# Kernel optimization log

Measured on AMD Instinct MI355X. Metric: run time of the kernel, lower is better.

The kernel has to match this reference:

```python
import jax, jax.numpy as jnp
import numpy as np

NUM_EMBEDDINGS = 1024
EMBEDDING_DIM = 256
COMMITMENT_COST = 0.25
DECAY = 0.99
EPSILON = 1e-05


def setup_inputs() -> dict:
    key = jax.random.key(0)
    k1, k2, k3 = jax.random.split(key, 3)
    z = jax.random.normal(k1, (32, EMBEDDING_DIM, 32, 32), dtype=jnp.float32)
    codebook = jax.random.normal(k2, (NUM_EMBEDDINGS, EMBEDDING_DIM), dtype=jnp.float32)
    ema_cluster_size = jnp.zeros((NUM_EMBEDDINGS,), dtype=jnp.float32)
    ema_dw = jax.random.normal(k3, (NUM_EMBEDDINGS, EMBEDDING_DIM), dtype=jnp.float32)
    return {"z": z, "codebook": codebook, "ema_cluster_size": ema_cluster_size, "ema_dw": ema_dw}


def reference(z, codebook, ema_cluster_size, ema_dw):
    K, D = codebook.shape
    # (B,C,H,W) -> (B,H,W,C)
    zp = jnp.transpose(z, (0, 2, 3, 1))
    z_flat = zp.reshape(-1, D)  # [N, D]
    N = z_flat.shape[0]

    # squared L2 distances to each code: [N, K]
    distances = (jnp.sum(z_flat ** 2, axis=1, keepdims=True)
                 + jnp.sum(codebook ** 2, axis=1)
                 - 2.0 * z_flat @ codebook.T)
    idx = jnp.argmin(distances, axis=1)  # [N]

    quantized = codebook[idx].reshape(zp.shape)  # [B,H,W,C]

    # training-mode EMA codebook update (one-hot scatter expressed as segment sums)
    counts = jax.ops.segment_sum(jnp.ones((N,), z_flat.dtype), idx, num_segments=K)  # encodings.sum(0)
    dw = jax.ops.segment_sum(z_flat, idx, num_segments=K)                            # encodings.T @ z_flat
    new_cluster_size = ema_cluster_size * DECAY + (1.0 - DECAY) * counts
    new_ema_dw = ema_dw * DECAY + (1.0 - DECAY) * dw
    n = jnp.sum(new_cluster_size)
    cluster_size = (new_cluster_size + EPSILON) / (n + K * EPSILON) * n
    new_codebook = new_ema_dw / cluster_size[:, None]

    commitment_loss = jnp.mean((zp - jax.lax.stop_gradient(quantized)) ** 2)
    loss = COMMITMENT_COST * commitment_loss

    # straight-through estimator
    quantized_st = zp + jax.lax.stop_gradient(quantized - zp)

    avg_probs = counts / N
    perplexity = jnp.exp(-jnp.sum(avg_probs * jnp.log(avg_probs + 1e-10)))

    quantized_out = jnp.transpose(quantized_st, (0, 3, 1, 2))  # back to (B,C,H,W)
    return (quantized_out, loss, perplexity, new_codebook, new_cluster_size, new_ema_dw)
```

## Files before the change

### kernel.cpp

```cpp
#include <hip/hip_runtime.h>
#include <cfloat>
#include <cstdint>

#define B_BATCH 32
#define D_DIM   256
#define HW      1024
#define N_POS   32768
#define K_CODES 1024
#define DECAY_F   0.99f
#define ONE_M_DECAY 0.01f
#define EPS_F   1e-5f

#define OUT_Q    0
#define OUT_LOSS 8388608
#define OUT_PERP 8388609
#define OUT_CB   8388610
#define OUT_NCS  8650754
#define OUT_EDW  8651778


#define WS_COUNTS  0
#define WS_LOSS    4096
#define WS_NTOT    4100
#define WS_MEMSET  4104
#define WS_CBNORM  4352
#define WS_OFFS    8448
#define WS_CURSOR  12544
#define WS_IDX     16640
#define WS_SORTED  147712
#define WS_CBHI    278784
#define WS_CBLO    803072
#define WS_PART    1327360
#define WS_SCODE   3424512
#define WS_TOTAL   3555584

typedef short s16x8 __attribute__((ext_vector_type(8)));
typedef float f32x4 __attribute__((ext_vector_type(4)));
typedef unsigned long long u64;

__device__ __forceinline__ ushort f2bf_rne(float x) {
    uint u = __float_as_uint(x);
    uint r = (u + 0x7FFF + ((u >> 16) & 1)) >> 16;
    return (ushort)r;
}
__device__ __forceinline__ float bf2f(ushort h) {
    return __uint_as_float(((uint)h) << 16);
}

__device__ __forceinline__ void gload16(const void* g, void* l) {
    __builtin_amdgcn_global_load_lds(
        (const __attribute__((address_space(1))) unsigned*)(uintptr_t)g,
        (__attribute__((address_space(3))) unsigned*)(uintptr_t)l, 16, 0, 0);
}

__global__ __launch_bounds__(256) void prep_kernel(const float* __restrict__ cb,
                                                   ushort* __restrict__ hi,
                                                   ushort* __restrict__ lo,
                                                   float* __restrict__ cbnorm) {
    int wave = threadIdx.x >> 6;
    int lane = threadIdx.x & 63;
    int k = blockIdx.x * 4 + wave;
    float4 v = *(const float4*)&cb[(size_t)k * D_DIM + lane * 4];
    ushort4 h, l;
    h.x = f2bf_rne(v.x); l.x = f2bf_rne(v.x - bf2f(h.x));
    h.y = f2bf_rne(v.y); l.y = f2bf_rne(v.y - bf2f(h.y));
    h.z = f2bf_rne(v.z); l.z = f2bf_rne(v.z - bf2f(h.z));
    h.w = f2bf_rne(v.w); l.w = f2bf_rne(v.w - bf2f(h.w));
    *(ushort4*)&hi[(size_t)k * D_DIM + lane * 4] = h;
    *(ushort4*)&lo[(size_t)k * D_DIM + lane * 4] = l;
    float s = v.x * v.x + v.y * v.y + v.z * v.z + v.w * v.w;
    #pragma unroll
    for (int off = 32; off >= 1; off >>= 1) s += __shfl_xor(s, off);
    if (lane == 0) cbnorm[k] = s;
}

__global__ __launch_bounds__(256) void ztrans_kernel(const float* __restrict__ z,
                                                     ushort* __restrict__ zhi,
                                                     ushort* __restrict__ zlo) {
    __shared__ float Zs[32][65];
    const int tid = threadIdx.x;
    const int n0  = blockIdx.x * 64;
    const int b   = n0 >> 10;
    const int hw0 = n0 & 1023;
    const float* zb = z + (size_t)b * (D_DIM * HW) + hw0;

    const int zn = tid & 63;
    const int zdb = (tid >> 6) * 8;
    const int n  = tid >> 2;
    const int dq = tid & 3;

    for (int d0 = 0; d0 < D_DIM; d0 += 32) {
        __syncthreads();
        #pragma unroll
        for (int j = 0; j < 8; ++j)
            Zs[zdb + j][zn] = zb[(size_t)(d0 + zdb + j) * HW + zn];
        __syncthreads();
        s16x8 hv, lv;
        #pragma unroll
        for (int j = 0; j < 8; ++j) {
            float f = Zs[dq * 8 + j][n];
            ushort hb = f2bf_rne(f);
            ushort lb = f2bf_rne(f - bf2f(hb));
            hv[j] = (short)hb;
            lv[j] = (short)lb;
        }
        *(s16x8*)&zhi[(size_t)(n0 + n) * D_DIM + d0 + dq * 8] = hv;
        *(s16x8*)&zlo[(size_t)(n0 + n) * D_DIM + d0 + dq * 8] = lv;
    }
}

__global__ __launch_bounds__(256) void argmin_gemm(const ushort* __restrict__ cbhi,
                                                   const ushort* __restrict__ cblo,
                                                   const ushort* __restrict__ zhi,
                                                   const ushort* __restrict__ zlo,
                                                   const float* __restrict__ cbnorm,
                                                   u64* __restrict__ partial) {
    __shared__ ushort lds[16384];
    __shared__ u64 kred[128][2];

    const int tid  = threadIdx.x;
    const int wave = tid >> 6;
    const int lane = tid & 63;
    const int col  = lane & 15;
    const int lg   = lane >> 4;
    const int mt = blockIdx.x & 7;
    const int pt = blockIdx.x >> 3;
    const int ch = wave & 1;
    const int ph = wave >> 1;

    const int r0  = tid >> 2;
    const int dch = (tid & 3) ^ ((r0 >> 1) & 3);
    const size_t eA0 = (size_t)(mt * 128 + r0) * D_DIM + dch * 8;
    const size_t eB0 = (size_t)(pt * 128 + r0) * D_DIM + dch * 8;
    const int ldsw = wave * 512;

    const int swz = (lg ^ ((col >> 1) & 3)) * 8;
    const int soffA = (ch * 64 + col) * 32 + swz;
    const int soffB = (ph * 64 + col) * 32 + swz;

    f32x4 acc[4][4];
    #pragma unroll
    for (int mi = 0; mi < 4; ++mi)
        #pragma unroll
        for (int ni = 0; ni < 4; ++ni) acc[mi][ni] = {0.f, 0.f, 0.f, 0.f};

    for (int s8 = 0; s8 < 8; ++s8) {
        const int d0 = s8 * 32;
        __syncthreads();
        gload16(cbhi + eA0 + d0,            &lds[0     + ldsw]);
        gload16(cbhi + eA0 + 64 * 256 + d0, &lds[2048  + ldsw]);
        gload16(cblo + eA0 + d0,            &lds[4096  + ldsw]);
        gload16(cblo + eA0 + 64 * 256 + d0, &lds[6144  + ldsw]);
        gload16(zhi  + eB0 + d0,            &lds[8192  + ldsw]);
        gload16(zhi  + eB0 + 64 * 256 + d0, &lds[10240 + ldsw]);
        gload16(zlo  + eB0 + d0,            &lds[12288 + ldsw]);
        gload16(zlo  + eB0 + 64 * 256 + d0, &lds[14336 + ldsw]);
        __syncthreads();

        s16x8 ah[4], al[4], bh[4], bl[4];
        #pragma unroll
        for (int mi = 0; mi < 4; ++mi) {
            int so = soffA + mi * 512;
            ah[mi] = *(const s16x8*)&lds[so];
            al[mi] = *(const s16x8*)&lds[4096 + so];
        }
        #pragma unroll
        for (int ni = 0; ni < 4; ++ni) {
            int so = soffB + ni * 512;
            bh[ni] = *(const s16x8*)&lds[8192 + so];
            bl[ni] = *(const s16x8*)&lds[12288 + so];
        }
        #pragma unroll
        for (int mi = 0; mi < 4; ++mi)
            #pragma unroll
            for (int ni = 0; ni < 4; ++ni) {
                acc[mi][ni] = __builtin_amdgcn_mfma_f32_16x16x32_bf16(ah[mi], bh[ni], acc[mi][ni], 0, 0, 0);
                acc[mi][ni] = __builtin_amdgcn_mfma_f32_16x16x32_bf16(ah[mi], bl[ni], acc[mi][ni], 0, 0, 0);
                acc[mi][ni] = __builtin_amdgcn_mfma_f32_16x16x32_bf16(al[mi], bh[ni], acc[mi][ni], 0, 0, 0);
            }
    }

    const int kbase = mt * 128 + ch * 64;
    u64 best[4] = {~0ull, ~0ull, ~0ull, ~0ull};
    #pragma unroll
    for (int mi = 0; mi < 4; ++mi) {
        float4 cn = *(const float4*)&cbnorm[kbase + mi * 16 + lg * 4];
        const float* cnp = (const float*)&cn;
        #pragma unroll
        for (int ni = 0; ni < 4; ++ni) {
            #pragma unroll
            for (int r = 0; r < 4; ++r) {
                float dist = cnp[r] - 2.f * acc[mi][ni][r];
                uint ub = __float_as_uint(dist);
                ub = ub ^ (uint)(((int)ub >> 31) | 0x80000000);
                u64 key = ((u64)ub << 32) | (uint)(kbase + mi * 16 + lg * 4 + r);
                if (key < best[ni]) best[ni] = key;
            }
        }
    }
    #pragma unroll
    for (int ni = 0; ni < 4; ++ni) {
        u64 o = __shfl_xor(best[ni], 16); if (o < best[ni]) best[ni] = o;
        o = __shfl_xor(best[ni], 32); if (o < best[ni]) best[ni] = o;
    }
    if (lane < 16) {
        #pragma unroll
        for (int ni = 0; ni < 4; ++ni)
            kred[ph * 64 + ni * 16 + lane][ch] = best[ni];
    }
    __syncthreads();
    if (tid < 128) {
        u64 a = kred[tid][0], b = kred[tid][1];
        partial[(size_t)(pt * 128 + tid) * 8 + mt] = a < b ? a : b;
    }
}

__global__ __launch_bounds__(256) void combine_kernel(const u64* __restrict__ partial,
                                                      int* __restrict__ idx,
                                                      float* __restrict__ counts) {
    __shared__ int hist[1024];
    const int tid = threadIdx.x;
    for (int j = tid; j < 1024; j += 256) hist[j] = 0;
    __syncthreads();
    int n = blockIdx.x * 256 + tid;
    const u64* p = partial + (size_t)n * 8;
    u64 m = p[0];
    #pragma unroll
    for (int j = 1; j < 8; ++j) { u64 v = p[j]; if (v < m) m = v; }
    int k = (int)(m & 1023u);
    idx[n] = k;
    atomicAdd(&hist[k], 1);
    __syncthreads();
    for (int j = tid; j < 1024; j += 256) {
        int c = hist[j];
        if (c) atomicAdd(&counts[j], (float)c);
    }
}

__global__ __launch_bounds__(1024) void small_kernel(const float* __restrict__ ema_cs,
                                                     const float* __restrict__ counts,
                                                     float* __restrict__ out_ncs,
                                                     float* __restrict__ out_perp,
                                                     float* __restrict__ ntot_ws,
                                                     int* __restrict__ offsets,
                                                     int* __restrict__ cursor) {
    __shared__ float s1[1024];
    __shared__ float s2[1024];
    __shared__ int   s3[1024];
    int k = threadIdx.x;
    float cnt = counts[k];
    float ncs = ema_cs[k] * DECAY_F + ONE_M_DECAY * cnt;
    out_ncs[k] = ncs;
    float p = cnt / (float)N_POS;
    s1[k] = ncs;
    s2[k] = p * logf(p + 1e-10f);
    int c = (int)cnt;
    s3[k] = c;
    __syncthreads();
    for (int off = 1; off < 1024; off <<= 1) {
        int v = (k >= off) ? s3[k - off] : 0;
        __syncthreads();
        s3[k] += v;
        __syncthreads();
    }
    int excl = s3[k] - c;
    offsets[k] = excl;
    cursor[k] = excl;
    for (int st = 512; st >= 1; st >>= 1) {
        if (k < st) { s1[k] += s1[k + st]; s2[k] += s2[k + st]; }
        __syncthreads();
    }
    if (k == 0) {
        ntot_ws[0] = s1[0];
        out_perp[0] = expf(-s2[0]);
    }
}

__global__ __launch_bounds__(256) void scatter_kernel(const int* __restrict__ idx,
                                                      int* __restrict__ cursor,
                                                      int* __restrict__ sorted,
                                                      int* __restrict__ scode) {
    __shared__ int hist[1024];
    __shared__ int base_s[1024];
    const int tid = threadIdx.x;
    for (int j = tid; j < 1024; j += 256) hist[j] = 0;
    __syncthreads();
    int n = blockIdx.x * 256 + tid;
    int k = idx[n];
    atomicAdd(&hist[k], 1);
    __syncthreads();
    for (int j = tid; j < 1024; j += 256) {
        int c = hist[j];
        if (c) base_s[j] = atomicAdd(&cursor[j], c);
        hist[j] = 0;
    }
    __syncthreads();
    int rank = atomicAdd(&hist[k], 1);
    int pos = base_s[k] + rank;
    sorted[pos] = n;
    scode[pos] = k;
}

#define DW_CHUNK 64
__global__ __launch_bounds__(256) void dw_chunk_kernel(const ushort* __restrict__ zhi,
                                                       const ushort* __restrict__ zlo,
                                                       const int* __restrict__ sorted,
                                                       const int* __restrict__ scode,
                                                       const int* __restrict__ offsets,
                                                       const float* __restrict__ counts,
                                                       float* __restrict__ dw) {
    __shared__ int sid[DW_CHUNK];
    __shared__ int sk[DW_CHUNK];
    const int tid = threadIdx.x;
    const int p0 = blockIdx.x * DW_CHUNK;
    if (tid < DW_CHUNK) {
        sid[tid] = sorted[p0 + tid];
        sk[tid]  = scode[p0 + tid];
    }
    __syncthreads();
    float acc = 0.f;
    int runstart = 0;
    #pragma unroll 4
    for (int i = 0; i < DW_CHUNK; ++i) {
        int id = sid[i];
        float zv = bf2f(zhi[(size_t)id * D_DIM + tid]) + bf2f(zlo[(size_t)id * D_DIM + tid]);
        acc += zv;
        bool end = (i == DW_CHUNK - 1) || (sk[i + 1] != sk[i]);
        if (end) {
            int k = sk[i];
            int off = offsets[k];
            int cnt = (int)counts[k];
            if (p0 + runstart == off && p0 + i == off + cnt - 1)
                dw[(size_t)k * D_DIM + tid] = acc;
            else
                atomicAdd(&dw[(size_t)k * D_DIM + tid], acc);
            acc = 0.f;
            runstart = i + 1;
        }
    }
}

__global__ __launch_bounds__(256) void fuse_kernel(const float* __restrict__ z,
                                                   const float* __restrict__ cb,
                                                   const int* __restrict__ idx,
                                                   float* __restrict__ outq,
                                                   float* __restrict__ lossacc) {
    __shared__ float Zs[32][65];
    __shared__ float Qs[32][65];
    __shared__ int kidx[64];
    __shared__ float red[256];

    const int tid = threadIdx.x;
    const int n0  = blockIdx.x * 64;
    const int b   = n0 >> 10;
    const int hw0 = n0 & 1023;
    const float* zb = z    + (size_t)b * (D_DIM * HW) + hw0;
    float*       ob = outq + (size_t)b * (D_DIM * HW) + hw0;

    if (tid < 64) kidx[tid] = idx[n0 + tid];

    const int zn = tid & 63;
    const int zdb = (tid >> 6) * 8;
    float loss = 0.f;

    for (int d0 = 0; d0 < D_DIM; d0 += 32) {
        __syncthreads();
        #pragma unroll
        for (int j = 0; j < 8; ++j)
            Zs[zdb + j][zn] = zb[(size_t)(d0 + zdb + j) * HW + zn];
        __syncthreads();

        #pragma unroll
        for (int h = 0; h < 2; ++h) {
            int s  = tid + 256 * h;
            int n  = s >> 3;
            int dq = s & 7;
            int k  = kidx[n];
            float4 q = *(const float4*)&cb[(size_t)k * D_DIM + d0 + dq * 4];
            float zx = Zs[dq * 4 + 0][n];
            float zy = Zs[dq * 4 + 1][n];
            float zz2 = Zs[dq * 4 + 2][n];
            float zw = Zs[dq * 4 + 3][n];
            Qs[dq * 4 + 0][n] = q.x;
            Qs[dq * 4 + 1][n] = q.y;
            Qs[dq * 4 + 2][n] = q.z;
            Qs[dq * 4 + 3][n] = q.w;
            float dx = zx - q.x, dy = zy - q.y, dz = zz2 - q.z, dww = zw - q.w;
            loss += dx * dx + dy * dy + dz * dz + dww * dww;
        }
        __syncthreads();

        #pragma unroll
        for (int j = 0; j < 8; ++j) {
            int v = tid + 256 * j;
            int d = v >> 6;
            int n = v & 63;
            float qq = Qs[d][n];
            float zval = Zs[d][n];
            ob[(size_t)(d0 + d) * HW + n] = zval + (qq - zval);
        }
    }

    red[tid] = loss;
    __syncthreads();
    for (int s2 = 128; s2 >= 1; s2 >>= 1) {
        if (tid < s2) red[tid] += red[tid + s2];
        __syncthreads();
    }
    if (tid == 0) atomicAdd(lossacc, red[0]);
}

__global__ __launch_bounds__(256) void finalize_rows(const float* __restrict__ ema_dw,
                                                     const float* __restrict__ out_ncs,
                                                     const float* __restrict__ ntot_ws,
                                                     const float* __restrict__ lossacc,
                                                     float* __restrict__ out_edw,
                                                     float* __restrict__ out_cb,
                                                     float* __restrict__ out_loss) {
    int k = blockIdx.x;
    int d = threadIdx.x;
    float ncs = out_ncs[k];
    float nt = ntot_ws[0];
    float csz = (ncs + EPS_F) / (nt + (float)K_CODES * EPS_F) * nt;
    size_t e = (size_t)k * D_DIM + d;
    float ed = ema_dw[e] * DECAY_F + ONE_M_DECAY * out_edw[e];
    out_edw[e] = ed;
    out_cb[e] = ed / csz;
    if (k == 0 && d == 0) out_loss[0] = 0.25f * lossacc[0] / 8388608.0f;
}

extern "C" void kernel_launch(void* const* d_in, const int* in_sizes, int n_in,
                              void* d_out, int out_size, void* d_ws, size_t ws_size,
                              hipStream_t stream) {
    const float* z       = (const float*)d_in[0];
    const float* cb      = (const float*)d_in[1];
    const float* ema_cs  = (const float*)d_in[2];
    const float* ema_dw  = (const float*)d_in[3];
    float* out = (float*)d_out;

    char* ws = (char*)d_ws;
    float* ws_counts = (float*)(ws + WS_COUNTS);
    float* ws_loss   = (float*)(ws + WS_LOSS);
    float* ws_ntot   = (float*)(ws + WS_NTOT);
    float* ws_cbnorm = (float*)(ws + WS_CBNORM);
    int*   ws_offs   = (int*)(ws + WS_OFFS);
    int*   ws_cursor = (int*)(ws + WS_CURSOR);
    int*   ws_idx    = (int*)(ws + WS_IDX);
    int*   ws_sorted = (int*)(ws + WS_SORTED);
    ushort* ws_cbhi  = (ushort*)(ws + WS_CBHI);
    ushort* ws_cblo  = (ushort*)(ws + WS_CBLO);
    u64*   ws_part   = (u64*)(ws + WS_PART);
    int*   ws_scode  = (int*)(ws + WS_SCODE);

    ushort* zhi = (ushort*)out;
    ushort* zlo = zhi + 8388608;

    hipMemsetAsync(d_ws, 0, WS_MEMSET, stream);
    hipMemsetAsync(out + OUT_EDW, 0, K_CODES * D_DIM * sizeof(float), stream);

    prep_kernel<<<K_CODES / 4, 256, 0, stream>>>(cb, ws_cbhi, ws_cblo, ws_cbnorm);
    ztrans_kernel<<<N_POS / 64, 256, 0, stream>>>(z, zhi, zlo);
    argmin_gemm<<<2048, 256, 0, stream>>>(ws_cbhi, ws_cblo, zhi, zlo, ws_cbnorm, ws_part);
    combine_kernel<<<N_POS / 256, 256, 0, stream>>>(ws_part, ws_idx, ws_counts);
    small_kernel<<<1, 1024, 0, stream>>>(ema_cs, ws_counts, out + OUT_NCS,
                                         out + OUT_PERP, ws_ntot, ws_offs, ws_cursor);
    scatter_kernel<<<N_POS / 256, 256, 0, stream>>>(ws_idx, ws_cursor, ws_sorted, ws_scode);
    dw_chunk_kernel<<<N_POS / DW_CHUNK, 256, 0, stream>>>(zhi, zlo, ws_sorted, ws_scode,
                                                          ws_offs, ws_counts, out + OUT_EDW);
    fuse_kernel<<<N_POS / 64, 256, 0, stream>>>(z, cb, ws_idx, out + OUT_Q, ws_loss);
    finalize_rows<<<K_CODES, 256, 0, stream>>>(ema_dw, out + OUT_NCS, ws_ntot, ws_loss,
                                               out + OUT_EDW, out + OUT_CB,
                                               out + OUT_LOSS);
}
```

Measured before the change: 234.4 us.

## Derive commitment loss from argmin distances and drop z reread in output pass

The commitment loss is now computed as the sum of ||z||^2 plus the minimum distance value taken from the argmin partials. This removes the need to reread z in the final output kernel, which now writes only the gathered codebook rows. Codebook prep and z transpose are merged into one launch. The memset for the dw accumulator is folded into the scatter kernel, and the GEMM block-index mapping is permuted, presumably for cache locality. The loss now depends on the bf16-split distance estimate plus the norm, which can change its rounding and risks cancellation error. The output no longer computes z + (q - z) exactly and writes q directly.

```diff
diff --git a/kernel.cpp b/kernel.cpp
--- a/kernel.cpp
+++ b/kernel.cpp
@@ -20,8 +20,8 @@
 
 
 #define WS_COUNTS  0
-#define WS_LOSS    4096
-#define WS_NTOT    4100
+#define WS_ZNORM   4096
+#define WS_BSUM    4100
 #define WS_MEMSET  4104
 #define WS_CBNORM  4352
 #define WS_OFFS    8448
@@ -53,32 +53,37 @@
         (__attribute__((address_space(3))) unsigned*)(uintptr_t)l, 16, 0, 0);
 }
 
-__global__ __launch_bounds__(256) void prep_kernel(const float* __restrict__ cb,
-                                                   ushort* __restrict__ hi,
-                                                   ushort* __restrict__ lo,
-                                                   float* __restrict__ cbnorm) {
-    int wave = threadIdx.x >> 6;
-    int lane = threadIdx.x & 63;
-    int k = blockIdx.x * 4 + wave;
-    float4 v = *(const float4*)&cb[(size_t)k * D_DIM + lane * 4];
-    ushort4 h, l;
-    h.x = f2bf_rne(v.x); l.x = f2bf_rne(v.x - bf2f(h.x));
-    h.y = f2bf_rne(v.y); l.y = f2bf_rne(v.y - bf2f(h.y));
-    h.z = f2bf_rne(v.z); l.z = f2bf_rne(v.z - bf2f(h.z));
-    h.w = f2bf_rne(v.w); l.w = f2bf_rne(v.w - bf2f(h.w));
-    *(ushort4*)&hi[(size_t)k * D_DIM + lane * 4] = h;
-    *(ushort4*)&lo[(size_t)k * D_DIM + lane * 4] = l;
-    float s = v.x * v.x + v.y * v.y + v.z * v.z + v.w * v.w;
-    #pragma unroll
-    for (int off = 32; off >= 1; off >>= 1) s += __shfl_xor(s, off);
-    if (lane == 0) cbnorm[k] = s;
-}
-
-__global__ __launch_bounds__(256) void ztrans_kernel(const float* __restrict__ z,
-                                                     ushort* __restrict__ zhi,
-                                                     ushort* __restrict__ zlo) {
+__global__ __launch_bounds__(256) void prep_ztrans(const float* __restrict__ z,
+                                                   const float* __restrict__ cb,
+                                                   ushort* __restrict__ zhi,
+                                                   ushort* __restrict__ zlo,
+                                                   ushort* __restrict__ cbhi,
+                                                   ushort* __restrict__ cblo,
+                                                   float* __restrict__ cbnorm,
+                                                   float* __restrict__ znorm_acc) {
     __shared__ float Zs[32][65];
+    __shared__ float red[256];
     const int tid = threadIdx.x;
+
+    if (blockIdx.x >= 512) {
+        int wave = tid >> 6;
+        int lane = tid & 63;
+        int k = (blockIdx.x - 512) * 4 + wave;
+        float4 v = *(const float4*)&cb[(size_t)k * D_DIM + lane * 4];
+        ushort4 h, l;
+        h.x = f2bf_rne(v.x); l.x = f2bf_rne(v.x - bf2f(h.x));
+        h.y = f2bf_rne(v.y); l.y = f2bf_rne(v.y - bf2f(h.y));
+        h.z = f2bf_rne(v.z); l.z = f2bf_rne(v.z - bf2f(h.z));
+        h.w = f2bf_rne(v.w); l.w = f2bf_rne(v.w - bf2f(h.w));
+        *(ushort4*)&cbhi[(size_t)k * D_DIM + lane * 4] = h;
+        *(ushort4*)&cblo[(size_t)k * D_DIM + lane * 4] = l;
+        float s = v.x * v.x + v.y * v.y + v.z * v.z + v.w * v.w;
+        #pragma unroll
+        for (int off = 32; off >= 1; off >>= 1) s += __shfl_xor(s, off);
+        if (lane == 0) cbnorm[k] = s;
+        return;
+    }
+
     const int n0  = blockIdx.x * 64;
     const int b   = n0 >> 10;
     const int hw0 = n0 & 1023;
@@ -88,6 +93,7 @@
     const int zdb = (tid >> 6) * 8;
     const int n  = tid >> 2;
     const int dq = tid & 3;
+    float zsum = 0.f;
 
     for (int d0 = 0; d0 < D_DIM; d0 += 32) {
         __syncthreads();
@@ -99,6 +105,7 @@
         #pragma unroll
         for (int j = 0; j < 8; ++j) {
             float f = Zs[dq * 8 + j][n];
+            zsum += f * f;
             ushort hb = f2bf_rne(f);
             ushort lb = f2bf_rne(f - bf2f(hb));
             hv[j] = (short)hb;
@@ -107,6 +114,13 @@
         *(s16x8*)&zhi[(size_t)(n0 + n) * D_DIM + d0 + dq * 8] = hv;
         *(s16x8*)&zlo[(size_t)(n0 + n) * D_DIM + d0 + dq * 8] = lv;
     }
+    red[tid] = zsum;
+    __syncthreads();
+    for (int s2 = 128; s2 >= 1; s2 >>= 1) {
+        if (tid < s2) red[tid] += red[tid + s2];
+        __syncthreads();
+    }
+    if (tid == 0) atomicAdd(znorm_acc, red[0]);
 }
 
 __global__ __launch_bounds__(256) void argmin_gemm(const ushort* __restrict__ cbhi,
@@ -123,8 +137,9 @@
     const int lane = tid & 63;
     const int col  = lane & 15;
     const int lg   = lane >> 4;
-    const int mt = blockIdx.x & 7;
-    const int pt = blockIdx.x >> 3;
+    const int blk = blockIdx.x;
+    const int mt = (blk >> 3) & 7;
+    const int pt = (blk & 7) | ((blk >> 6) << 3);
     const int ch = wave & 1;
     const int ph = wave >> 1;
 
@@ -217,8 +232,10 @@
 
 __global__ __launch_bounds__(256) void combine_kernel(const u64* __restrict__ partial,
                                                       int* __restrict__ idx,
-                                                      float* __restrict__ counts) {
+                                                      float* __restrict__ counts,
+                                                      float* __restrict__ bsum_acc) {
     __shared__ int hist[1024];
+    __shared__ float red[256];
     const int tid = threadIdx.x;
     for (int j = tid; j < 1024; j += 256) hist[j] = 0;
     __syncthreads();
@@ -230,7 +247,15 @@
     int k = (int)(m & 1023u);
     idx[n] = k;
     atomicAdd(&hist[k], 1);
-    __syncthreads();
+    uint ub = (uint)(m >> 32);
+    uint u = (ub & 0x80000000u) ? (ub ^ 0x80000000u) : ~ub;
+    red[tid] = __uint_as_float(u);
+    __syncthreads();
+    for (int s2 = 128; s2 >= 1; s2 >>= 1) {
+        if (tid < s2) red[tid] += red[tid + s2];
+        __syncthreads();
+    }
+    if (tid == 0) atomicAdd(bsum_acc, red[0]);
     for (int j = tid; j < 1024; j += 256) {
         int c = hist[j];
         if (c) atomicAdd(&counts[j], (float)c);
@@ -239,8 +264,11 @@
 
 __global__ __launch_bounds__(1024) void small_kernel(const float* __restrict__ ema_cs,
                                                      const float* __restrict__ counts,
+                                                     const float* __restrict__ znorm,
+                                                     const float* __restrict__ bsum,
                                                      float* __restrict__ out_ncs,
                                                      float* __restrict__ out_perp,
+                                                     float* __restrict__ out_loss,
                                                      float* __restrict__ ntot_ws,
                                                      int* __restrict__ offsets,
                                                      int* __restrict__ cursor) {
@@ -273,16 +301,24 @@
     if (k == 0) {
         ntot_ws[0] = s1[0];
         out_perp[0] = expf(-s2[0]);
+        out_loss[0] = 0.25f * (znorm[0] + bsum[0]) / 8388608.0f;
     }
 }
 
 __global__ __launch_bounds__(256) void scatter_kernel(const int* __restrict__ idx,
                                                       int* __restrict__ cursor,
                                                       int* __restrict__ sorted,
-                                                      int* __restrict__ scode) {
+                                                      int* __restrict__ scode,
+                                                      float* __restrict__ dw_zero) {
     __shared__ int hist[1024];
     __shared__ int base_s[1024];
     const int tid = threadIdx.x;
+    {
+        float4 z4 = {0.f, 0.f, 0.f, 0.f};
+        size_t e = ((size_t)blockIdx.x * 256 + tid) * 8;
+        *(float4*)&dw_zero[e] = z4;
+        *(float4*)&dw_zero[e + 4] = z4;
+    }
     for (int j = tid; j < 1024; j += 256) hist[j] = 0;
     __syncthreads();
     int n = blockIdx.x * 256 + tid;
@@ -340,36 +376,21 @@
     }
 }
 
-__global__ __launch_bounds__(256) void fuse_kernel(const float* __restrict__ z,
-                                                   const float* __restrict__ cb,
-                                                   const int* __restrict__ idx,
-                                                   float* __restrict__ outq,
-                                                   float* __restrict__ lossacc) {
-    __shared__ float Zs[32][65];
+__global__ __launch_bounds__(256) void fuse_lite(const float* __restrict__ cb,
+                                                 const int* __restrict__ idx,
+                                                 float* __restrict__ outq) {
     __shared__ float Qs[32][65];
     __shared__ int kidx[64];
-    __shared__ float red[256];
-
     const int tid = threadIdx.x;
     const int n0  = blockIdx.x * 64;
     const int b   = n0 >> 10;
     const int hw0 = n0 & 1023;
-    const float* zb = z    + (size_t)b * (D_DIM * HW) + hw0;
-    float*       ob = outq + (size_t)b * (D_DIM * HW) + hw0;
+    float* ob = outq + (size_t)b * (D_DIM * HW) + hw0;
 
     if (tid < 64) kidx[tid] = idx[n0 + tid];
 
-    const int zn = tid & 63;
-    const int zdb = (tid >> 6) * 8;
-    float loss = 0.f;
-
     for (int d0 = 0; d0 < D_DIM; d0 += 32) {
         __syncthreads();
-        #pragma unroll
-        for (int j = 0; j < 8; ++j)
-            Zs[zdb + j][zn] = zb[(size_t)(d0 + zdb + j) * HW + zn];
-        __syncthreads();
-
         #pragma unroll
         for (int h = 0; h < 2; ++h) {
             int s  = tid + 256 * h;
@@ -377,46 +398,27 @@
             int dq = s & 7;
             int k  = kidx[n];
             float4 q = *(const float4*)&cb[(size_t)k * D_DIM + d0 + dq * 4];
-            float zx = Zs[dq * 4 + 0][n];
-            float zy = Zs[dq * 4 + 1][n];
-            float zz2 = Zs[dq * 4 + 2][n];
-            float zw = Zs[dq * 4 + 3][n];
             Qs[dq * 4 + 0][n] = q.x;
             Qs[dq * 4 + 1][n] = q.y;
             Qs[dq * 4 + 2][n] = q.z;
             Qs[dq * 4 + 3][n] = q.w;
-            float dx = zx - q.x, dy = zy - q.y, dz = zz2 - q.z, dww = zw - q.w;
-            loss += dx * dx + dy * dy + dz * dz + dww * dww;
-        }
-        __syncthreads();
-
+        }
+        __syncthreads();
         #pragma unroll
         for (int j = 0; j < 8; ++j) {
             int v = tid + 256 * j;
             int d = v >> 6;
             int n = v & 63;
-            float qq = Qs[d][n];
-            float zval = Zs[d][n];
-            ob[(size_t)(d0 + d) * HW + n] = zval + (qq - zval);
-        }
-    }
-
-    red[tid] = loss;
-    __syncthreads();
-    for (int s2 = 128; s2 >= 1; s2 >>= 1) {
-        if (tid < s2) red[tid] += red[tid + s2];
-        __syncthreads();
-    }
-    if (tid == 0) atomicAdd(lossacc, red[0]);
+            ob[(size_t)(d0 + d) * HW + n] = Qs[d][n];
+        }
+    }
 }
 
 __global__ __launch_bounds__(256) void finalize_rows(const float* __restrict__ ema_dw,
                                                      const float* __restrict__ out_ncs,
                                                      const float* __restrict__ ntot_ws,
-                                                     const float* __restrict__ lossacc,
                                                      float* __restrict__ out_edw,
-                                                     float* __restrict__ out_cb,
-                                                     float* __restrict__ out_loss) {
+                                                     float* __restrict__ out_cb) {
     int k = blockIdx.x;
     int d = threadIdx.x;
     float ncs = out_ncs[k];
@@ -426,7 +428,6 @@
     float ed = ema_dw[e] * DECAY_F + ONE_M_DECAY * out_edw[e];
     out_edw[e] = ed;
     out_cb[e] = ed / csz;
-    if (k == 0 && d == 0) out_loss[0] = 0.25f * lossacc[0] / 8388608.0f;
 }
 
 extern "C" void kernel_launch(void* const* d_in, const int* in_sizes, int n_in,
@@ -440,8 +441,8 @@
 
     char* ws = (char*)d_ws;
     float* ws_counts = (float*)(ws + WS_COUNTS);
-    float* ws_loss   = (float*)(ws + WS_LOSS);
-    float* ws_ntot   = (float*)(ws + WS_NTOT);
+    float* ws_znorm  = (float*)(ws + WS_ZNORM);
+    float* ws_bsum   = (float*)(ws + WS_BSUM);
     float* ws_cbnorm = (float*)(ws + WS_CBNORM);
     int*   ws_offs   = (int*)(ws + WS_OFFS);
     int*   ws_cursor = (int*)(ws + WS_CURSOR);
@@ -456,19 +457,20 @@
     ushort* zlo = zhi + 8388608;
 
     hipMemsetAsync(d_ws, 0, WS_MEMSET, stream);
-    hipMemsetAsync(out + OUT_EDW, 0, K_CODES * D_DIM * sizeof(float), stream);
-
-    prep_kernel<<<K_CODES / 4, 256, 0, stream>>>(cb, ws_cbhi, ws_cblo, ws_cbnorm);
-    ztrans_kernel<<<N_POS / 64, 256, 0, stream>>>(z, zhi, zlo);
+
+    prep_ztrans<<<768, 256, 0, stream>>>(z, cb, zhi, zlo, ws_cbhi, ws_cblo,
+                                         ws_cbnorm, ws_znorm);
     argmin_gemm<<<2048, 256, 0, stream>>>(ws_cbhi, ws_cblo, zhi, zlo, ws_cbnorm, ws_part);
-    combine_kernel<<<N_POS / 256, 256, 0, stream>>>(ws_part, ws_idx, ws_counts);
-    small_kernel<<<1, 1024, 0, stream>>>(ema_cs, ws_counts, out + OUT_NCS,
-                                         out + OUT_PERP, ws_ntot, ws_offs, ws_cursor);
-    scatter_kernel<<<N_POS / 256, 256, 0, stream>>>(ws_idx, ws_cursor, ws_sorted, ws_scode);
+    combine_kernel<<<N_POS / 256, 256, 0, stream>>>(ws_part, ws_idx, ws_counts, ws_bsum);
+    small_kernel<<<1, 1024, 0, stream>>>(ema_cs, ws_counts, ws_znorm, ws_bsum,
+                                         out + OUT_NCS, out + OUT_PERP, out + OUT_LOSS,
+                                         (float*)(ws + WS_ZNORM) + 1024, ws_offs, ws_cursor);
+    scatter_kernel<<<N_POS / 256, 256, 0, stream>>>(ws_idx, ws_cursor, ws_sorted,
+                                                    ws_scode, out + OUT_EDW);
     dw_chunk_kernel<<<N_POS / DW_CHUNK, 256, 0, stream>>>(zhi, zlo, ws_sorted, ws_scode,
                                                           ws_offs, ws_counts, out + OUT_EDW);
-    fuse_kernel<<<N_POS / 64, 256, 0, stream>>>(z, cb, ws_idx, out + OUT_Q, ws_loss);
-    finalize_rows<<<K_CODES, 256, 0, stream>>>(ema_dw, out + OUT_NCS, ws_ntot, ws_loss,
-                                               out + OUT_EDW, out + OUT_CB,
-                                               out + OUT_LOSS);
-}
+    fuse_lite<<<N_POS / 64, 256, 0, stream>>>(cb, ws_idx, out + OUT_Q);
+    finalize_rows<<<K_CODES, 256, 0, stream>>>(ema_dw, out + OUT_NCS,
+                                               (float*)(ws + WS_ZNORM) + 1024,
+                                               out + OUT_EDW, out + OUT_CB);
+}
```

New measurement: 213.9 us. 8.8% less time.
